# Optimization experiments

Measured on AMD Instinct MI355X. Metric: run time of the kernel, lower is better.

## Reference

```python
import jax, jax.numpy as jnp
import numpy as np

LN_EPS = 1e-9
NEG_INF = float(-2**32 + 1)


def setup_inputs() -> dict:
    key = jax.random.key(0)
    k1, k2 = jax.random.split(key)
    B, T, C = 64, 1024, 256
    x = jax.random.normal(k1, (B, T, C), dtype=jnp.float32)
    key_masks = jax.random.randint(k2, (B, 1, T), 0, 2) > 0  # bool [B,1,T]
    gamma = jnp.ones((C,), dtype=jnp.float32)
    beta = jnp.zeros((C,), dtype=jnp.float32)
    return {"x": x, "key_masks": key_masks, "gamma": gamma, "beta": beta}


def reference(x, key_masks, gamma, beta):
    # x: [B,T,C]; key_masks: [B,1,T] bool; gamma/beta: [C]
    B, T, C = x.shape
    inv_scale = 1.0 / np.sqrt(C).astype(np.float32)
    # DotAttention: QK^T scaled -> [B,T,T]
    align = jnp.einsum('btc,bsc->bts', x, x) * inv_scale
    # key padding mask (broadcast over query axis)
    align = jnp.where(key_masks, align, NEG_INF)
    # future binding: causal lower-triangular mask
    causal = jnp.tril(jnp.ones((T, T), dtype=bool))
    align = jnp.where(causal[None, :, :], align, NEG_INF)
    attn = jax.nn.softmax(align, axis=-1)  # dropout_rate=0 / inference -> identity
    out = jnp.einsum('bts,bsc->btc', attn, x)  # [B,T,C]
    # LayerNorm over last axis
    mu = jnp.mean(out, axis=-1, keepdims=True)
    var = jnp.mean(jnp.square(out - mu), axis=-1, keepdims=True)
    out = gamma * (out - mu) * jax.lax.rsqrt(var + LN_EPS) + beta
    # reduce_mean over time axis, keepdims
    return jnp.mean(out, axis=1, keepdims=True)  # [B,1,C]
```

## Files before the change

kernel.cpp:

```cpp
#include <hip/hip_runtime.h>

#define B_   64
#define T_   1024
#define C_   256
#define NEGF (-4294967295.0f)
#define LN_EPS 1e-9f

typedef short  short8 __attribute__((ext_vector_type(8)));
typedef float  f32x4  __attribute__((ext_vector_type(4)));

union S8 { short8 v; unsigned int w[4]; };

__device__ __forceinline__ unsigned int pk2(float x, float y) {
  unsigned a = __float_as_uint(x); a = (a + 0x7fffu + ((a >> 16) & 1u)) >> 16;
  unsigned b = __float_as_uint(y); b = (b + 0x7fffu + ((b >> 16) & 1u)) >> 16;
  return a | (b << 16);
}

__device__ __forceinline__ void async16(const void* g, void* l) {
  __builtin_amdgcn_global_load_lds(
      (const __attribute__((address_space(1))) void*)g,
      (__attribute__((address_space(3))) void*)l,
      16, 0, 0);
}


__global__ void detect_kernel(const unsigned int* __restrict__ mw,
                              int* __restrict__ flag) {
  int idx = blockIdx.x * 256 + threadIdx.x;
  if (mw[idx] > 1u) atomicOr(flag, 1);
}

__global__ void finalize_kernel(const float* __restrict__ accum,
                                float* __restrict__ out) {
  int idx = blockIdx.x * 256 + threadIdx.x;
  out[idx] = accum[idx] * (1.0f / T_);
}

__global__ __launch_bounds__(256) void convert_kv(const float* __restrict__ x,
                                                  const unsigned int* __restrict__ mw,
                                                  const int* __restrict__ flag,
                                                  short* __restrict__ xk,
                                                  short* __restrict__ xv,
                                                  float* __restrict__ colsum,
                                                  float2* __restrict__ sb) {
  __shared__ float Xt[32 * 256];
  __shared__ __align__(16) short Vt[8192];
  __shared__ float csum[4][256];
  const int blk = blockIdx.x, b = blk >> 5, tt = blk & 31;
  const int tid = threadIdx.x;
  const float* xt = x + (size_t)(b * 1024 + tt * 32) * 256;

  if (tid < 32) {
    int idx = b * 1024 + tt * 32 + tid;
    int f = *flag;
    unsigned int w = mw[f ? (idx >> 2) : idx];
    unsigned int v = f ? ((w >> ((idx & 3) * 8)) & 0xffu) : w;
    sb[idx] = v ? make_float2(0.0625f, 0.f) : make_float2(0.f, NEGF);
  }

#pragma unroll
  for (int u = 0; u < 4; ++u) {
    int id = u * 256 + tid;
    int row = id >> 5, ck = id & 31;
    const float* src = xt + row * 256 + ck * 8;
    float4 a  = *(const float4*)src;
    float4 c4 = *(const float4*)(src + 4);
    *(float4*)&Xt[row * 256 + ck * 8]     = a;
    *(float4*)&Xt[row * 256 + ck * 8 + 4] = c4;
    S8 s; s.w[0] = pk2(a.x, a.y);  s.w[1] = pk2(a.z, a.w);
          s.w[2] = pk2(c4.x, c4.y); s.w[3] = pk2(c4.z, c4.w);
    *(short8*)(xk + (size_t)(b * 1024 + tt * 32 + row) * 256 + ((ck ^ row) << 3)) = s.v;
  }
  __syncthreads();

  const int ck = tid >> 6, clo = tid & 63;
#pragma unroll
  for (int g = 0; g < 4; ++g) {
    int c = g * 64 + clo;
    float vs[8]; float s = 0.f;
#pragma unroll
    for (int e = 0; e < 8; ++e) { vs[e] = Xt[(ck * 8 + e) * 256 + c]; s += vs[e]; }
    S8 o;
    o.w[0] = pk2(vs[0], vs[1]); o.w[1] = pk2(vs[2], vs[3]);
    o.w[2] = pk2(vs[4], vs[5]); o.w[3] = pk2(vs[6], vs[7]);
    *(short8*)&Vt[c * 32 + (((ck ^ ((c >> 1) & 3)) & 3) << 3)] = o.v;
    csum[ck][c] = s;
  }
  __syncthreads();

  {
    float4* vo = (float4*)(xv + (size_t)(b * 32 + tt) * 8192);
    const float4* vi = (const float4*)Vt;
#pragma unroll
    for (int r = 0; r < 4; ++r) vo[r * 256 + tid] = vi[r * 256 + tid];
    float s = csum[0][tid] + csum[1][tid] + csum[2][tid] + csum[3][tid];
    atomicAdd(&colsum[b * 256 + tid], s);
  }
}

__device__ __forceinline__ void finalize_tile(
    f32x4* Oa, float m, float l, int b, int quad, int r,
    const float* __restrict__ colsum, const float* __restrict__ gamma,
    const float* __restrict__ beta, float* __restrict__ accum)
{
  float mr[4], li[4];
#pragma unroll
  for (int reg = 0; reg < 4; ++reg) {
    mr[reg] = __shfl(m, quad * 4 + reg, 64);
    float lr = __shfl(l, quad * 4 + reg, 64);
    li[reg] = 1.f / lr;
  }
#pragma unroll
  for (int ct = 0; ct < 16; ++ct) {
    float cs = colsum[b * C_ + ct * 16 + r] * (1.0f / T_);
#pragma unroll
    for (int reg = 0; reg < 4; ++reg)
      Oa[ct][reg] = (mr[reg] < -1.0e9f) ? cs : Oa[ct][reg] * li[reg];
  }
  float ts[16];
#pragma unroll
  for (int ct = 0; ct < 16; ++ct) ts[ct] = 0.f;
#pragma unroll
  for (int reg = 0; reg < 4; ++reg) {
    float s2 = 0.f;
#pragma unroll
    for (int ct = 0; ct < 16; ++ct) s2 += Oa[ct][reg];
    s2 += __shfl_xor(s2, 1, 64); s2 += __shfl_xor(s2, 2, 64);
    s2 += __shfl_xor(s2, 4, 64); s2 += __shfl_xor(s2, 8, 64);
    float mu = s2 * (1.0f / C_);
    float sq = 0.f;
#pragma unroll
    for (int ct = 0; ct < 16; ++ct) { float d = Oa[ct][reg] - mu; sq += d * d; }
    sq += __shfl_xor(sq, 1, 64); sq += __shfl_xor(sq, 2, 64);
    sq += __shfl_xor(sq, 4, 64); sq += __shfl_xor(sq, 8, 64);
    float rstd = rsqrtf(sq * (1.0f / C_) + LN_EPS);
#pragma unroll
    for (int ct = 0; ct < 16; ++ct) {
      int c = ct * 16 + r;
      ts[ct] += gamma[c] * (Oa[ct][reg] - mu) * rstd + beta[c];
    }
  }
#pragma unroll
  for (int ct = 0; ct < 16; ++ct) {
    ts[ct] += __shfl_xor(ts[ct], 16, 64);
    ts[ct] += __shfl_xor(ts[ct], 32, 64);
  }
  if (quad == 0) {
#pragma unroll
    for (int ct = 0; ct < 16; ++ct)
      atomicAdd(&accum[b * C_ + ct * 16 + r], ts[ct]);
  }
}

__global__ __launch_bounds__(512, 2) void flash5(
    const short* __restrict__ xk,
    const short* __restrict__ xv,
    const float2* __restrict__ sb,
    const float* __restrict__ gamma,
    const float* __restrict__ beta,
    const float* __restrict__ colsum,
    float* __restrict__ accum)
{
  __shared__ __align__(16) short KsD[2][64 * 256];
  __shared__ __align__(16) short VtD[2][2 * 256 * 32];

  const int i0 = blockIdx.x;
  const int x8 = i0 & 7;
  const int s  = i0 >> 3;
  const int b  = x8 + 8 * (s & 7);
  const int t  = s >> 3;

  const int tid  = threadIdx.x;
  const int w    = tid >> 6;
  const int lane = tid & 63;
  const int quad = lane >> 4;
  const int r    = lane & 15;

  const int h0len = 2 * (t + 1);

  int qt   = t;
  int n0   = qt * 128 + w * 16;
  int qrow = n0 + r;
  short8 qf[8];
  {
    const short* qp = xk + (size_t)(b * 1024 + qrow) * 256;
#pragma unroll
    for (int ks = 0; ks < 8; ++ks)
      qf[ks] = *(const short8*)(qp + (((ks * 4 + quad) ^ (qrow & 31)) << 3));
  }
  f32x4 Oa[16];
#pragma unroll
  for (int ct = 0; ct < 16; ++ct) Oa[ct] = (f32x4){0.f, 0.f, 0.f, 0.f};
  float m = NEGF, l = 0.f;

  {
    const short* gk = xk + (size_t)(b * 1024) * 256;
    const short* gv = xv + (size_t)(b * 32) * 8192;
#pragma unroll
    for (int u = 0; u < 4; ++u) {
      int seg = w * 4 + u;
      async16(gk + seg * 512 + lane * 8, &KsD[0][seg * 512]);
      async16(gv + seg * 512 + lane * 8, &VtD[0][seg * 512]);
    }
  }
  __syncthreads();

  for (int idx = 0; idx < 18; ++idx) {
    const int ibuf = idx & 1;
    if (idx < 17) {
      const int nt2 = (idx + 1 < h0len) ? (idx + 1) : (17 - (idx + 1));
      const short* gk = xk + (size_t)(b * 1024 + nt2 * 64) * 256;
      const short* gv = xv + (size_t)(b * 32 + nt2 * 2) * 8192;
#pragma unroll
      for (int u = 0; u < 4; ++u) {
        int seg = w * 4 + u;
        async16(gk + seg * 512 + lane * 8, &KsD[1 - ibuf][seg * 512]);
        async16(gv + seg * 512 + lane * 8, &VtD[1 - ibuf][seg * 512]);
      }
    }

    const int kt  = (idx < h0len) ? idx : (17 - idx);
    const int ktb = kt * 64;
    if (ktb <= n0 + 15) {
      float sc[16];
#pragma unroll
      for (int mt = 0; mt < 4; ++mt) {
        f32x4 acc = (f32x4){0.f, 0.f, 0.f, 0.f};
        const int row = mt * 16 + r;
#pragma unroll
        for (int ks = 0; ks < 8; ++ks) {
          short8 af = *(short8*)&KsD[ibuf][row * 256 + (((ks * 4 + quad) ^ (row & 31)) << 3)];
          acc = __builtin_amdgcn_mfma_f32_16x16x32_bf16(af, qf[ks], acc, 0, 0, 0);
        }
        const int j0 = ktb + mt * 16 + quad * 4;
        float4 sA = *(const float4*)(sb + (size_t)b * 1024 + j0);
        float4 sB = *(const float4*)(sb + (size_t)b * 1024 + j0 + 2);
        sc[mt * 4 + 0] = acc[0] * sA.x + sA.y;
        sc[mt * 4 + 1] = acc[1] * sA.z + sA.w;
        sc[mt * 4 + 2] = acc[2] * sB.x + sB.y;
        sc[mt * 4 + 3] = acc[3] * sB.z + sB.w;
      }
      if (ktb + 63 > n0) {
#pragma unroll
        for (int k2 = 0; k2 < 16; ++k2) {
          int j = ktb + (k2 >> 2) * 16 + quad * 4 + (k2 & 3);
          if (j > qrow) sc[k2] = NEGF;
        }
      }

      float mx = sc[0];
#pragma unroll
      for (int k2 = 1; k2 < 16; ++k2) mx = fmaxf(mx, sc[k2]);
      mx = fmaxf(mx, __shfl_xor(mx, 16, 64));
      mx = fmaxf(mx, __shfl_xor(mx, 32, 64));
      if (__ballot(mx > m + 8.f)) {
        const float mnew  = fmaxf(m, mx);
        const float alpha = __expf(m - mnew);
        float ar[4];
#pragma unroll
        for (int reg = 0; reg < 4; ++reg) ar[reg] = __shfl(alpha, quad * 4 + reg, 64);
#pragma unroll
        for (int ct = 0; ct < 16; ++ct) {
          Oa[ct][0] *= ar[0]; Oa[ct][1] *= ar[1];
          Oa[ct][2] *= ar[2]; Oa[ct][3] *= ar[3];
        }
        l *= alpha;
        m = mnew;
      }
      float p[16], ps = 0.f;
#pragma unroll
      for (int k2 = 0; k2 < 16; ++k2) { p[k2] = __expf(sc[k2] - m); ps += p[k2]; }
      ps += __shfl_xor(ps, 16, 64);
      ps += __shfl_xor(ps, 32, 64);
      l += ps;

      S8 pf[2];
#pragma unroll
      for (int hh = 0; hh < 2; ++hh) {
        unsigned q0 = pk2(p[hh * 8 + 0], p[hh * 8 + 1]);
        unsigned q1 = pk2(p[hh * 8 + 2], p[hh * 8 + 3]);
        unsigned q2 = pk2(p[hh * 8 + 4], p[hh * 8 + 5]);
        unsigned q3 = pk2(p[hh * 8 + 6], p[hh * 8 + 7]);
        int s0l = ((quad & 1) << 5) + r, s1l = s0l + 16;
        unsigned u0 = __shfl((int)q0, s0l, 64), u1 = __shfl((int)q1, s0l, 64);
        unsigned u2 = __shfl((int)q2, s0l, 64), u3 = __shfl((int)q3, s0l, 64);
        unsigned v0 = __shfl((int)q0, s1l, 64), v1 = __shfl((int)q1, s1l, 64);
        unsigned v2 = __shfl((int)q2, s1l, 64), v3 = __shfl((int)q3, s1l, 64);
        bool hi = quad >= 2;
        pf[hh].w[0] = hi ? u2 : u0; pf[hh].w[1] = hi ? u3 : u1;
        pf[hh].w[2] = hi ? v2 : v0; pf[hh].w[3] = hi ? v3 : v1;
      }

#pragma unroll
      for (int ct = 0; ct < 16; ++ct) {
        int c = ct * 16 + r;
        int cs_off = c * 32 + (((quad ^ ((c >> 1) & 3)) & 3) << 3);
        short8 b0 = *(short8*)&VtD[ibuf][cs_off];
        short8 b1 = *(short8*)&VtD[ibuf][8192 + cs_off];
        Oa[ct] = __builtin_amdgcn_mfma_f32_16x16x32_bf16(pf[0].v, b0, Oa[ct], 0, 0, 0);
        Oa[ct] = __builtin_amdgcn_mfma_f32_16x16x32_bf16(pf[1].v, b1, Oa[ct], 0, 0, 0);
      }
    }

    if (idx == h0len - 1) {
      finalize_tile(Oa, m, l, b, quad, r, colsum, gamma, beta, accum);
      qt = 7 - t;
      n0 = qt * 128 + w * 16;
      qrow = n0 + r;
      const short* qp = xk + (size_t)(b * 1024 + qrow) * 256;
#pragma unroll
      for (int ks = 0; ks < 8; ++ks)
        qf[ks] = *(const short8*)(qp + (((ks * 4 + quad) ^ (qrow & 31)) << 3));
#pragma unroll
      for (int ct = 0; ct < 16; ++ct) Oa[ct] = (f32x4){0.f, 0.f, 0.f, 0.f};
      m = NEGF; l = 0.f;
    }

    __syncthreads();
  }

  finalize_tile(Oa, m, l, b, quad, r, colsum, gamma, beta, accum);
}


extern "C" void kernel_launch(void* const* d_in, const int* in_sizes, int n_in,
                              void* d_out, int out_size, void* d_ws, size_t ws_size,
                              hipStream_t stream) {
  const float* x     = (const float*)d_in[0];
  const void*  km    = d_in[1];
  const float* gamma = (const float*)d_in[2];
  const float* beta  = (const float*)d_in[3];
  float* out = (float*)d_out;

  const size_t off_sb = 131200;
  const size_t off_xk = 655616;
  const size_t off_xv = off_xk + 33554432;

  float*  accum  = (float*)d_ws;
  float*  colsum = (float*)((char*)d_ws + 65536);
  int*    flag   = (int*)((char*)d_ws + 131072);
  float2* sb     = (float2*)((char*)d_ws + off_sb);
  short*  xk     = (short*)((char*)d_ws + off_xk);
  short*  xv     = (short*)((char*)d_ws + off_xv);

  hipMemsetAsync(d_ws, 0, 131136, stream);
  detect_kernel<<<64, 256, 0, stream>>>((const unsigned int*)km, flag);
  convert_kv<<<B_ * 32, 256, 0, stream>>>(x, (const unsigned int*)km, flag,
                                          xk, xv, colsum, sb);
  flash5<<<256, 512, 0, stream>>>(xk, xv, sb, gamma, beta, colsum, accum);
  finalize_kernel<<<B_ * C_ / 256, 256, 0, stream>>>(accum, out);
}
```

Baseline: 172.3 us.

## Fold finalize into flash atomics, transpose bf16 in convert, add MFMA priority hints

Result: no change. 172.3 us (+0.0%).

```diff
diff --git a/kernel.cpp b/kernel.cpp
--- a/kernel.cpp
+++ b/kernel.cpp
@@ -29,12 +29,6 @@
                               int* __restrict__ flag) {
   int idx = blockIdx.x * 256 + threadIdx.x;
   if (mw[idx] > 1u) atomicOr(flag, 1);
-}
-
-__global__ void finalize_kernel(const float* __restrict__ accum,
-                                float* __restrict__ out) {
-  int idx = blockIdx.x * 256 + threadIdx.x;
-  out[idx] = accum[idx] * (1.0f / T_);
 }
 
 __global__ __launch_bounds__(256) void convert_kv(const float* __restrict__ x,
@@ -44,9 +38,9 @@
                                                   short* __restrict__ xv,
                                                   float* __restrict__ colsum,
                                                   float2* __restrict__ sb) {
-  __shared__ float Xt[32 * 256];
+  __shared__ __align__(16) short Kb[32 * 256];
   __shared__ __align__(16) short Vt[8192];
-  __shared__ float csum[4][256];
+  __shared__ float csum[8][256];
   const int blk = blockIdx.x, b = blk >> 5, tt = blk & 31;
   const int tid = threadIdx.x;
   const float* xt = x + (size_t)(b * 1024 + tt * 32) * 256;
@@ -59,33 +53,47 @@
     sb[idx] = v ? make_float2(0.0625f, 0.f) : make_float2(0.f, NEGF);
   }
 
+  float myc[8];
+#pragma unroll
+  for (int e = 0; e < 8; ++e) myc[e] = 0.f;
+  const int ck = tid & 31;
 #pragma unroll
   for (int u = 0; u < 4; ++u) {
     int id = u * 256 + tid;
-    int row = id >> 5, ck = id & 31;
+    int row = id >> 5;
     const float* src = xt + row * 256 + ck * 8;
     float4 a  = *(const float4*)src;
     float4 c4 = *(const float4*)(src + 4);
-    *(float4*)&Xt[row * 256 + ck * 8]     = a;
-    *(float4*)&Xt[row * 256 + ck * 8 + 4] = c4;
+    myc[0] += a.x;  myc[1] += a.y;  myc[2] += a.z;  myc[3] += a.w;
+    myc[4] += c4.x; myc[5] += c4.y; myc[6] += c4.z; myc[7] += c4.w;
     S8 s; s.w[0] = pk2(a.x, a.y);  s.w[1] = pk2(a.z, a.w);
           s.w[2] = pk2(c4.x, c4.y); s.w[3] = pk2(c4.z, c4.w);
     *(short8*)(xk + (size_t)(b * 1024 + tt * 32 + row) * 256 + ((ck ^ row) << 3)) = s.v;
+    *(short8*)&Kb[row * 256 + ((ck ^ (row & 7)) << 3)] = s.v;
+  }
+  {
+    const int rg = tid >> 5;
+#pragma unroll
+    for (int e = 0; e < 8; ++e) csum[rg][ck * 8 + e] = myc[e];
   }
   __syncthreads();
 
-  const int ck = tid >> 6, clo = tid & 63;
+  const int ck2 = tid >> 6, clo = tid & 63;
 #pragma unroll
   for (int g = 0; g < 4; ++g) {
     int c = g * 64 + clo;
-    float vs[8]; float s = 0.f;
-#pragma unroll
-    for (int e = 0; e < 8; ++e) { vs[e] = Xt[(ck * 8 + e) * 256 + c]; s += vs[e]; }
+    unsigned short sv[8];
+#pragma unroll
+    for (int e = 0; e < 8; ++e) {
+      int k = ck2 * 8 + e;
+      sv[e] = (unsigned short)Kb[k * 256 + (((c >> 3) ^ (k & 7)) << 3) + (c & 7)];
+    }
     S8 o;
-    o.w[0] = pk2(vs[0], vs[1]); o.w[1] = pk2(vs[2], vs[3]);
-    o.w[2] = pk2(vs[4], vs[5]); o.w[3] = pk2(vs[6], vs[7]);
-    *(short8*)&Vt[c * 32 + (((ck ^ ((c >> 1) & 3)) & 3) << 3)] = o.v;
-    csum[ck][c] = s;
+    o.w[0] = (unsigned)sv[0] | ((unsigned)sv[1] << 16);
+    o.w[1] = (unsigned)sv[2] | ((unsigned)sv[3] << 16);
+    o.w[2] = (unsigned)sv[4] | ((unsigned)sv[5] << 16);
+    o.w[3] = (unsigned)sv[6] | ((unsigned)sv[7] << 16);
+    *(short8*)&Vt[c * 32 + (((ck2 ^ ((c >> 1) & 3)) & 3) << 3)] = o.v;
   }
   __syncthreads();
 
@@ -94,7 +102,8 @@
     const float4* vi = (const float4*)Vt;
 #pragma unroll
     for (int r = 0; r < 4; ++r) vo[r * 256 + tid] = vi[r * 256 + tid];
-    float s = csum[0][tid] + csum[1][tid] + csum[2][tid] + csum[3][tid];
+    float s = csum[0][tid] + csum[1][tid] + csum[2][tid] + csum[3][tid]
+            + csum[4][tid] + csum[5][tid] + csum[6][tid] + csum[7][tid];
     atomicAdd(&colsum[b * 256 + tid], s);
   }
 }
@@ -102,7 +111,7 @@
 __device__ __forceinline__ void finalize_tile(
     f32x4* Oa, float m, float l, int b, int quad, int r,
     const float* __restrict__ colsum, const float* __restrict__ gamma,
-    const float* __restrict__ beta, float* __restrict__ accum)
+    const float* __restrict__ beta, float* __restrict__ out)
 {
   float mr[4], li[4];
 #pragma unroll
@@ -149,7 +158,7 @@
   if (quad == 0) {
 #pragma unroll
     for (int ct = 0; ct < 16; ++ct)
-      atomicAdd(&accum[b * C_ + ct * 16 + r], ts[ct]);
+      atomicAdd(&out[b * C_ + ct * 16 + r], ts[ct] * (1.0f / T_));
   }
 }
 
@@ -160,7 +169,7 @@
     const float* __restrict__ gamma,
     const float* __restrict__ beta,
     const float* __restrict__ colsum,
-    float* __restrict__ accum)
+    float* __restrict__ out)
 {
   __shared__ __align__(16) short KsD[2][64 * 256];
   __shared__ __align__(16) short VtD[2][2 * 256 * 32];
@@ -224,6 +233,7 @@
     const int ktb = kt * 64;
     if (ktb <= n0 + 15) {
       float sc[16];
+      __builtin_amdgcn_s_setprio(1);
 #pragma unroll
       for (int mt = 0; mt < 4; ++mt) {
         f32x4 acc = (f32x4){0.f, 0.f, 0.f, 0.f};
@@ -241,6 +251,7 @@
         sc[mt * 4 + 2] = acc[2] * sB.x + sB.y;
         sc[mt * 4 + 3] = acc[3] * sB.z + sB.w;
       }
+      __builtin_amdgcn_s_setprio(0);
       if (ktb + 63 > n0) {
 #pragma unroll
         for (int k2 = 0; k2 < 16; ++k2) {
@@ -292,6 +303,7 @@
         pf[hh].w[2] = hi ? v2 : v0; pf[hh].w[3] = hi ? v3 : v1;
       }
 
+      __builtin_amdgcn_s_setprio(1);
 #pragma unroll
       for (int ct = 0; ct < 16; ++ct) {
         int c = ct * 16 + r;
@@ -301,10 +313,11 @@
         Oa[ct] = __builtin_amdgcn_mfma_f32_16x16x32_bf16(pf[0].v, b0, Oa[ct], 0, 0, 0);
         Oa[ct] = __builtin_amdgcn_mfma_f32_16x16x32_bf16(pf[1].v, b1, Oa[ct], 0, 0, 0);
       }
+      __builtin_amdgcn_s_setprio(0);
     }
 
     if (idx == h0len - 1) {
-      finalize_tile(Oa, m, l, b, quad, r, colsum, gamma, beta, accum);
+      finalize_tile(Oa, m, l, b, quad, r, colsum, gamma, beta, out);
       qt = 7 - t;
       n0 = qt * 128 + w * 16;
       qrow = n0 + r;
@@ -320,7 +333,7 @@
     __syncthreads();
   }
 
-  finalize_tile(Oa, m, l, b, quad, r, colsum, gamma, beta, accum);
+  finalize_tile(Oa, m, l, b, quad, r, colsum, gamma, beta, out);
 }
 
 
@@ -337,7 +350,6 @@
   const size_t off_xk = 655616;
   const size_t off_xv = off_xk + 33554432;
 
-  float*  accum  = (float*)d_ws;
   float*  colsum = (float*)((char*)d_ws + 65536);
   int*    flag   = (int*)((char*)d_ws + 131072);
   float2* sb     = (float2*)((char*)d_ws + off_sb);
@@ -345,9 +357,9 @@
   short*  xv     = (short*)((char*)d_ws + off_xv);
 
   hipMemsetAsync(d_ws, 0, 131136, stream);
+  hipMemsetAsync(d_out, 0, out_size, stream);
   detect_kernel<<<64, 256, 0, stream>>>((const unsigned int*)km, flag);
   convert_kv<<<B_ * 32, 256, 0, stream>>>(x, (const unsigned int*)km, flag,
                                           xk, xv, colsum, sb);
-  flash5<<<256, 512, 0, stream>>>(xk, xv, sb, gamma, beta, colsum, accum);
-  finalize_kernel<<<B_ * C_ / 256, 256, 0, stream>>>(accum, out);
-}
+  flash5<<<256, 512, 0, stream>>>(xk, xv, sb, gamma, beta, colsum, out);
+}
```
